# Performance work log

Measured on AMD Instinct MI355X. Metric: run time of the kernel, lower is better.

The kernel has to match this reference:

```python
import jax, jax.numpy as jnp
import numpy as np

TEMPERATURE = 0.2
EPS = 1e-10

def setup_inputs() -> dict:
    key = jax.random.key(0)
    x = jax.random.normal(key, (8, 1024, 64, 64), dtype=jnp.float32)
    return {"x": x}

def reference(x):
    B, C, H, W = x.shape
    xf = x.reshape(B, C, H * W)                      # [B, C, HW]
    dot = jnp.einsum('bcn,bdn->bcd', xf, xf) / TEMPERATURE  # [B, C, C]
    logits = jax.nn.softmax(dot, axis=-1)
    diag = jnp.diagonal(logits, axis1=-2, axis2=-1)  # [B, C]
    loss = -jnp.log(diag + EPS)
    return jnp.mean(loss)
```

## Files before the change

### kernel.cpp

```cpp
#include <hip/hip_runtime.h>
#include <hip/hip_bf16.h>

#define BATCH 8
#define CCH 1024
#define NHW 4096
#define SCALE 5.0f
#define ROWS (BATCH * CCH)

typedef unsigned char u8;
typedef unsigned int u32;
typedef __attribute__((ext_vector_type(4))) float float4v;
typedef __attribute__((ext_vector_type(4))) u32 uint4v;

__device__ __forceinline__ void async_load16(const void* gsrc, void* ldst) {
    __builtin_amdgcn_global_load_lds(
        (__attribute__((address_space(1))) void*)gsrc,
        (__attribute__((address_space(3))) void*)ldst,
        16, 0, 0);
}

__device__ __forceinline__ u32 pk4_fp8(float a, float b, float c, float d) {
    u32 v = __builtin_amdgcn_cvt_pk_fp8_f32(a, b, 0, false);
    v = __builtin_amdgcn_cvt_pk_fp8_f32(c, d, v, true);
    return v;
}

__device__ __forceinline__ float ssq4_fp8(u32 q) {
    float d0 = __builtin_amdgcn_cvt_f32_fp8(q, 0);
    float d1 = __builtin_amdgcn_cvt_f32_fp8(q, 1);
    float d2 = __builtin_amdgcn_cvt_f32_fp8(q, 2);
    float d3 = __builtin_amdgcn_cvt_f32_fp8(q, 3);
    return d0 * d0 + d1 * d1 + d2 * d2 + d3 * d3;
}

template <bool CONVERT>
__global__ __launch_bounds__(256) void prep_kernel(const float* __restrict__ x,
                                                   u8* __restrict__ xq,
                                                   float* __restrict__ diag,
                                                   float* __restrict__ l_acc) {
    const int row = blockIdx.x;
    const int tid = threadIdx.x;
    const float* src = x + (size_t)row * NHW;
    float ssum = 0.f;
#pragma unroll
    for (int p = 0; p < 4; ++p) {
        const int idx = p * 1024 + tid * 4;
        float4 v = *(const float4*)(src + idx);
        const u32 q = pk4_fp8(v.x, v.y, v.z, v.w);
        ssum += ssq4_fp8(q);
        if (CONVERT) *(u32*)(xq + (size_t)row * NHW + idx) = q;
    }
#pragma unroll
    for (int m = 1; m < 64; m <<= 1) ssum += __shfl_xor(ssum, m);
    __shared__ float red[4];
    if ((tid & 63) == 0) red[tid >> 6] = ssum;
    __syncthreads();
    if (tid == 0) {
        diag[row] = (red[0] + red[1] + red[2] + red[3]) * SCALE;
        l_acc[row] = 0.f;
    }
}

template <bool QSRC>
__global__ __launch_bounds__(256) void gram_kernel(const u8* __restrict__ Xq,
                                                   const float* __restrict__ Xf,
                                                   const float* __restrict__ diag,
                                                   float* __restrict__ l_acc,
                                                   float* __restrict__ num) {
    __shared__ __align__(16) u8 As[2][16384];
    __shared__ __align__(16) u8 Bs[2][8192];

    const int bid = blockIdx.x;
    const int b = bid & 7;
    const int t = bid >> 3;

    int bi = 0;
#pragma unroll
    for (int i = 7; i >= 1; --i) {
        if (t >= i * (17 - i)) { bi = i; break; }
    }
    const int bj2 = 2 * bi + (t - bi * (17 - bi));
    const bool aliasB = (bj2 == 2 * bi) || (bj2 == 2 * bi + 1);

    const int tid  = threadIdx.x;
    const int lane = tid & 63;
    const int w    = tid >> 6;
    const int wm   = w >> 1;
    const int wn   = w & 1;

    const int st_r  = lane >> 3;
    const int st_kc = (lane & 7) ^ st_r;

    const u8*    pA  = nullptr; const u8*    pB  = nullptr;
    const float* pAf = nullptr; const float* pBf = nullptr;
    if (QSRC) {
        const u8* baseX = Xq + (size_t)b * CCH * NHW;
        pA = baseX + (size_t)(bi * 128 + w * 32 + st_r) * NHW + st_kc * 16;
        pB = baseX + (size_t)(bj2 * 64 + w * 16 + st_r) * NHW + st_kc * 16;
    } else {
        const float* baseXf = Xf + (size_t)b * CCH * NHW;
        pAf = baseXf + (size_t)(bi * 128 + w * 32 + st_r) * NHW + st_kc * 16;
        pBf = baseXf + (size_t)(bj2 * 64 + w * 16 + st_r) * NHW + st_kc * 16;
    }

    float4v acc[4][2] = {};

    auto stage = [&](int buf, int K0) {
        if (QSRC) {
#pragma unroll
            for (int t8 = 0; t8 < 4; ++t8)
                async_load16(pA + (size_t)(t8 * 8) * NHW + K0,
                             As[buf] + (size_t)(w * 32 + t8 * 8) * 128);
            if (!aliasB) {
#pragma unroll
                for (int t8 = 0; t8 < 2; ++t8)
                    async_load16(pB + (size_t)(t8 * 8) * NHW + K0,
                                 Bs[buf] + (size_t)(w * 16 + t8 * 8) * 128);
            }
        } else {
#pragma unroll
            for (int t8 = 0; t8 < 4; ++t8) {
                const float* s = pAf + (size_t)(t8 * 8) * NHW + K0;
                float4 f0 = *(const float4*)(s);
                float4 f1 = *(const float4*)(s + 4);
                float4 f2 = *(const float4*)(s + 8);
                float4 f3 = *(const float4*)(s + 12);
                uint4v d;
                d.x = pk4_fp8(f0.x, f0.y, f0.z, f0.w);
                d.y = pk4_fp8(f1.x, f1.y, f1.z, f1.w);
                d.z = pk4_fp8(f2.x, f2.y, f2.z, f2.w);
                d.w = pk4_fp8(f3.x, f3.y, f3.z, f3.w);
                *(uint4v*)(As[buf] + (size_t)(w * 32 + t8 * 8 + st_r) * 128 + (lane & 7) * 16) = d;
            }
            if (!aliasB) {
#pragma unroll
                for (int t8 = 0; t8 < 2; ++t8) {
                    const float* s = pBf + (size_t)(t8 * 8) * NHW + K0;
                    float4 f0 = *(const float4*)(s);
                    float4 f1 = *(const float4*)(s + 4);
                    float4 f2 = *(const float4*)(s + 8);
                    float4 f3 = *(const float4*)(s + 12);
                    uint4v d;
                    d.x = pk4_fp8(f0.x, f0.y, f0.z, f0.w);
                    d.y = pk4_fp8(f1.x, f1.y, f1.z, f1.w);
                    d.z = pk4_fp8(f2.x, f2.y, f2.z, f2.w);
                    d.w = pk4_fp8(f3.x, f3.y, f3.z, f3.w);
                    *(uint4v*)(Bs[buf] + (size_t)(w * 16 + t8 * 8 + st_r) * 128 + (lane & 7) * 16) = d;
                }
            }
        }
    };

    stage(0, 0);
    __syncthreads();

    for (int i = 0; i < NHW / 128; ++i) {
        const int cur = i & 1;
        const int K0n = (i + 1) * 128;
        if (K0n < NHW) stage(cur ^ 1, K0n);

        const u8* Ab = As[cur];
        const u8* Bb = aliasB ? (Ab + (size_t)(bj2 - 2 * bi) * 64 * 128) : Bs[cur];
        const int q  = lane >> 4;
        const int rl = lane & 15;
#pragma unroll
        for (int s = 0; s < 4; ++s) {
            const int cbase = 2 * s + (q >> 1);
            const int boff  = (int)((cbase ^ (rl & 7)) * 16 + (q & 1) * 8);
            long af[4], bf[2];
#pragma unroll
            for (int mt = 0; mt < 4; ++mt)
                af[mt] = *(const long*)(Ab + (size_t)(wm * 64 + mt * 16 + rl) * 128 + boff);
#pragma unroll
            for (int nt = 0; nt < 2; ++nt)
                bf[nt] = *(const long*)(Bb + (size_t)(wn * 32 + nt * 16 + rl) * 128 + boff);
#pragma unroll
            for (int mt = 0; mt < 4; ++mt)
#pragma unroll
                for (int nt = 0; nt < 2; ++nt)
                    acc[mt][nt] = __builtin_amdgcn_mfma_f32_16x16x32_fp8_fp8(af[mt], bf[nt], acc[mt][nt], 0, 0, 0);
        }
        __syncthreads();
    }

    const int q  = lane >> 4;
    const int cl = lane & 15;
    const int rowbase = bi * 128 + wm * 64;
    const int colbase = bj2 * 64 + wn * 32;
    const float* dgb = diag + b * CCH;
    float* lb = l_acc + b * CCH;

#pragma unroll
    for (int mt = 0; mt < 4; ++mt) {
#pragma unroll
        for (int reg = 0; reg < 4; ++reg) {
            const int gr = rowbase + mt * 16 + q * 4 + reg;
            const float dg = dgb[gr];
            float s = 0.f;
#pragma unroll
            for (int nt = 0; nt < 2; ++nt) {
                const int gc = colbase + nt * 16 + cl;
                const float e = __expf(acc[mt][nt][reg] * SCALE - dg);
                if (gr <= gc) s += e;
                if (gr == gc) num[b * CCH + gr] = e;
            }
            s += __shfl_xor(s, 1);
            s += __shfl_xor(s, 2);
            s += __shfl_xor(s, 4);
            s += __shfl_xor(s, 8);
            if (cl == 0) atomicAdd(lb + gr, s);
        }
    }

#pragma unroll
    for (int nt = 0; nt < 2; ++nt) {
        const int gc = colbase + nt * 16 + cl;
        const float dgc = dgb[gc];
        float s = 0.f;
#pragma unroll
        for (int mt = 0; mt < 4; ++mt) {
#pragma unroll
            for (int reg = 0; reg < 4; ++reg) {
                const int gr = rowbase + mt * 16 + q * 4 + reg;
                if (gr < gc) s += __expf(acc[mt][nt][reg] * SCALE - dgc);
            }
        }
        s += __shfl_xor(s, 16);
        s += __shfl_xor(s, 32);
        if (lane < 16) atomicAdd(lb + gc, s);
    }
}

__global__ __launch_bounds__(1024) void finalize_kernel(const float* __restrict__ l_acc,
                                                        const float* __restrict__ num,
                                                        float* __restrict__ out) {
    const int tid = threadIdx.x;
    float s = 0.f;
    for (int r = tid; r < ROWS; r += 1024) {
        const float d = num[r] / l_acc[r];
        s += -__logf(d + 1e-10f);
    }
#pragma unroll
    for (int m = 1; m < 64; m <<= 1) s += __shfl_xor(s, m);
    __shared__ float red[16];
    if ((tid & 63) == 0) red[tid >> 6] = s;
    __syncthreads();
    if (tid == 0) {
        float tot = 0.f;
#pragma unroll
        for (int i = 0; i < 16; ++i) tot += red[i];
        out[0] = tot * (1.0f / (float)ROWS);
    }
}

extern "C" void kernel_launch(void* const* d_in, const int* in_sizes, int n_in,
                              void* d_out, int out_size, void* d_ws, size_t ws_size,
                              hipStream_t stream) {
    const float* x = (const float*)d_in[0];
    float* out = (float*)d_out;

    const size_t xq_bytes   = (size_t)BATCH * CCH * NHW;
    const size_t stat_bytes = (size_t)ROWS * 4;
    const bool fast = ws_size >= xq_bytes + 3 * stat_bytes;

    const int ntiles = 72;

    if (fast) {
        u8*    xq    = (u8*)d_ws;
        float* diag  = (float*)((char*)d_ws + xq_bytes);
        float* l_acc = diag + ROWS;
        float* num   = l_acc + ROWS;
        prep_kernel<true><<<ROWS, 256, 0, stream>>>(x, xq, diag, l_acc);
        gram_kernel<true><<<BATCH * ntiles, 256, 0, stream>>>(xq, nullptr, diag, l_acc, num);
        finalize_kernel<<<1, 1024, 0, stream>>>(l_acc, num, out);
    } else {
        float* diag  = (float*)d_ws;
        float* l_acc = diag + ROWS;
        float* num   = l_acc + ROWS;
        prep_kernel<false><<<ROWS, 256, 0, stream>>>(x, nullptr, diag, l_acc);
        gram_kernel<false><<<BATCH * ntiles, 256, 0, stream>>>(nullptr, x, diag, l_acc, num);
        finalize_kernel<<<1, 1024, 0, stream>>>(l_acc, num, out);
    }
}
```

Before: 241.0 us.

## Use persistent atomic-ticket gram kernel and fuse finalize via last-block reduction

The gram kernel becomes persistent: a fixed grid of 512 blocks pulls tile tickets from a global atomic counter until all 576 tiles are processed, instead of launching one block per tile. The separate finalize kernel is removed; the last block to finish, detected with a second counter and threadfences, computes the final mean loss. This is meant to cut one kernel launch and smooth load balance across the tail, at the cost of per-tile atomics and a serialized final reduction inside one block.

```diff
diff --git a/kernel.cpp b/kernel.cpp
--- a/kernel.cpp
+++ b/kernel.cpp
@@ -6,6 +6,9 @@
 #define NHW 4096
 #define SCALE 5.0f
 #define ROWS (BATCH * CCH)
+#define NTILES 72
+#define NTICK (BATCH * NTILES)
+#define GRID_G 512
 
 typedef unsigned char u8;
 typedef unsigned int u32;
@@ -37,7 +40,8 @@
 __global__ __launch_bounds__(256) void prep_kernel(const float* __restrict__ x,
                                                    u8* __restrict__ xq,
                                                    float* __restrict__ diag,
-                                                   float* __restrict__ l_acc) {
+                                                   float* __restrict__ l_acc,
+                                                   int* __restrict__ counters) {
     const int row = blockIdx.x;
     const int tid = threadIdx.x;
     const float* src = x + (size_t)row * NHW;
@@ -58,6 +62,7 @@
     if (tid == 0) {
         diag[row] = (red[0] + red[1] + red[2] + red[3]) * SCALE;
         l_acc[row] = 0.f;
+        if (row == 0) { counters[0] = 0; counters[1] = 0; }
     }
 }
 
@@ -66,21 +71,13 @@
                                                    const float* __restrict__ Xf,
                                                    const float* __restrict__ diag,
                                                    float* __restrict__ l_acc,
-                                                   float* __restrict__ num) {
+                                                   float* __restrict__ num,
+                                                   int* __restrict__ counters,
+                                                   float* __restrict__ out) {
     __shared__ __align__(16) u8 As[2][16384];
     __shared__ __align__(16) u8 Bs[2][8192];
-
-    const int bid = blockIdx.x;
-    const int b = bid & 7;
-    const int t = bid >> 3;
-
-    int bi = 0;
-#pragma unroll
-    for (int i = 7; i >= 1; --i) {
-        if (t >= i * (17 - i)) { bi = i; break; }
-    }
-    const int bj2 = 2 * bi + (t - bi * (17 - bi));
-    const bool aliasB = (bj2 == 2 * bi) || (bj2 == 2 * bi + 1);
+    __shared__ int s_ticket;
+    __shared__ float s_red[4];
 
     const int tid  = threadIdx.x;
     const int lane = tid & 63;
@@ -91,51 +88,53 @@
     const int st_r  = lane >> 3;
     const int st_kc = (lane & 7) ^ st_r;
 
-    const u8*    pA  = nullptr; const u8*    pB  = nullptr;
-    const float* pAf = nullptr; const float* pBf = nullptr;
-    if (QSRC) {
-        const u8* baseX = Xq + (size_t)b * CCH * NHW;
-        pA = baseX + (size_t)(bi * 128 + w * 32 + st_r) * NHW + st_kc * 16;
-        pB = baseX + (size_t)(bj2 * 64 + w * 16 + st_r) * NHW + st_kc * 16;
-    } else {
-        const float* baseXf = Xf + (size_t)b * CCH * NHW;
-        pAf = baseXf + (size_t)(bi * 128 + w * 32 + st_r) * NHW + st_kc * 16;
-        pBf = baseXf + (size_t)(bj2 * 64 + w * 16 + st_r) * NHW + st_kc * 16;
-    }
-
-    float4v acc[4][2] = {};
-
-    auto stage = [&](int buf, int K0) {
+    const int q_  = lane >> 4;
+    const int cl  = lane & 15;
+
+    for (;;) {
+        if (tid == 0) s_ticket = atomicAdd(counters + 0, 1);
+        __syncthreads();
+        const int tk = s_ticket;
+        if (tk >= NTICK) break;
+
+        const int b = tk & 7;
+        const int t = tk >> 3;
+        int bi = 0;
+#pragma unroll
+        for (int i = 7; i >= 1; --i) {
+            if (t >= i * (17 - i)) { bi = i; break; }
+        }
+        const int bj2 = 2 * bi + (t - bi * (17 - bi));
+        const bool aliasB = (bj2 == 2 * bi) || (bj2 == 2 * bi + 1);
+
+        const u8*    pA  = nullptr; const u8*    pB  = nullptr;
+        const float* pAf = nullptr; const float* pBf = nullptr;
         if (QSRC) {
-#pragma unroll
-            for (int t8 = 0; t8 < 4; ++t8)
-                async_load16(pA + (size_t)(t8 * 8) * NHW + K0,
-                             As[buf] + (size_t)(w * 32 + t8 * 8) * 128);
-            if (!aliasB) {
-#pragma unroll
-                for (int t8 = 0; t8 < 2; ++t8)
-                    async_load16(pB + (size_t)(t8 * 8) * NHW + K0,
-                                 Bs[buf] + (size_t)(w * 16 + t8 * 8) * 128);
-            }
+            const u8* baseX = Xq + (size_t)b * CCH * NHW;
+            pA = baseX + (size_t)(bi * 128 + w * 32 + st_r) * NHW + st_kc * 16;
+            pB = baseX + (size_t)(bj2 * 64 + w * 16 + st_r) * NHW + st_kc * 16;
         } else {
-#pragma unroll
-            for (int t8 = 0; t8 < 4; ++t8) {
-                const float* s = pAf + (size_t)(t8 * 8) * NHW + K0;
-                float4 f0 = *(const float4*)(s);
-                float4 f1 = *(const float4*)(s + 4);
-                float4 f2 = *(const float4*)(s + 8);
-                float4 f3 = *(const float4*)(s + 12);
-                uint4v d;
-                d.x = pk4_fp8(f0.x, f0.y, f0.z, f0.w);
-                d.y = pk4_fp8(f1.x, f1.y, f1.z, f1.w);
-                d.z = pk4_fp8(f2.x, f2.y, f2.z, f2.w);
-                d.w = pk4_fp8(f3.x, f3.y, f3.z, f3.w);
-                *(uint4v*)(As[buf] + (size_t)(w * 32 + t8 * 8 + st_r) * 128 + (lane & 7) * 16) = d;
-            }
-            if (!aliasB) {
-#pragma unroll
-                for (int t8 = 0; t8 < 2; ++t8) {
-                    const float* s = pBf + (size_t)(t8 * 8) * NHW + K0;
+            const float* baseXf = Xf + (size_t)b * CCH * NHW;
+            pAf = baseXf + (size_t)(bi * 128 + w * 32 + st_r) * NHW + st_kc * 16;
+            pBf = baseXf + (size_t)(bj2 * 64 + w * 16 + st_r) * NHW + st_kc * 16;
+        }
+
+        auto stage = [&](int buf, int K0) {
+            if (QSRC) {
+#pragma unroll
+                for (int t8 = 0; t8 < 4; ++t8)
+                    async_load16(pA + (size_t)(t8 * 8) * NHW + K0,
+                                 As[buf] + (size_t)(w * 32 + t8 * 8) * 128);
+                if (!aliasB) {
+#pragma unroll
+                    for (int t8 = 0; t8 < 2; ++t8)
+                        async_load16(pB + (size_t)(t8 * 8) * NHW + K0,
+                                     Bs[buf] + (size_t)(w * 16 + t8 * 8) * 128);
+                }
+            } else {
+#pragma unroll
+                for (int t8 = 0; t8 < 4; ++t8) {
+                    const float* s = pAf + (size_t)(t8 * 8) * NHW + K0;
                     float4 f0 = *(const float4*)(s);
                     float4 f1 = *(const float4*)(s + 4);
                     float4 f2 = *(const float4*)(s + 8);
@@ -145,111 +144,126 @@
                     d.y = pk4_fp8(f1.x, f1.y, f1.z, f1.w);
                     d.z = pk4_fp8(f2.x, f2.y, f2.z, f2.w);
                     d.w = pk4_fp8(f3.x, f3.y, f3.z, f3.w);
-                    *(uint4v*)(Bs[buf] + (size_t)(w * 16 + t8 * 8 + st_r) * 128 + (lane & 7) * 16) = d;
-                }
-            }
-        }
-    };
-
-    stage(0, 0);
-    __syncthreads();
-
-    for (int i = 0; i < NHW / 128; ++i) {
-        const int cur = i & 1;
-        const int K0n = (i + 1) * 128;
-        if (K0n < NHW) stage(cur ^ 1, K0n);
-
-        const u8* Ab = As[cur];
-        const u8* Bb = aliasB ? (Ab + (size_t)(bj2 - 2 * bi) * 64 * 128) : Bs[cur];
-        const int q  = lane >> 4;
-        const int rl = lane & 15;
-#pragma unroll
-        for (int s = 0; s < 4; ++s) {
-            const int cbase = 2 * s + (q >> 1);
-            const int boff  = (int)((cbase ^ (rl & 7)) * 16 + (q & 1) * 8);
-            long af[4], bf[2];
-#pragma unroll
-            for (int mt = 0; mt < 4; ++mt)
-                af[mt] = *(const long*)(Ab + (size_t)(wm * 64 + mt * 16 + rl) * 128 + boff);
-#pragma unroll
-            for (int nt = 0; nt < 2; ++nt)
-                bf[nt] = *(const long*)(Bb + (size_t)(wn * 32 + nt * 16 + rl) * 128 + boff);
-#pragma unroll
-            for (int mt = 0; mt < 4; ++mt)
+                    *(uint4v*)(As[buf] + (size_t)(w * 32 + t8 * 8 + st_r) * 128 + (lane & 7) * 16) = d;
+                }
+                if (!aliasB) {
+#pragma unroll
+                    for (int t8 = 0; t8 < 2; ++t8) {
+                        const float* s = pBf + (size_t)(t8 * 8) * NHW + K0;
+                        float4 f0 = *(const float4*)(s);
+                        float4 f1 = *(const float4*)(s + 4);
+                        float4 f2 = *(const float4*)(s + 8);
+                        float4 f3 = *(const float4*)(s + 12);
+                        uint4v d;
+                        d.x = pk4_fp8(f0.x, f0.y, f0.z, f0.w);
+                        d.y = pk4_fp8(f1.x, f1.y, f1.z, f1.w);
+                        d.z = pk4_fp8(f2.x, f2.y, f2.z, f2.w);
+                        d.w = pk4_fp8(f3.x, f3.y, f3.z, f3.w);
+                        *(uint4v*)(Bs[buf] + (size_t)(w * 16 + t8 * 8 + st_r) * 128 + (lane & 7) * 16) = d;
+                    }
+                }
+            }
+        };
+
+        float4v acc[4][2] = {};
+
+        stage(0, 0);
+        __syncthreads();
+
+        for (int i = 0; i < NHW / 128; ++i) {
+            const int cur = i & 1;
+            const int K0n = (i + 1) * 128;
+            if (K0n < NHW) stage(cur ^ 1, K0n);
+
+            const u8* Ab = As[cur];
+            const u8* Bb = aliasB ? (Ab + (size_t)(bj2 - 2 * bi) * 64 * 128) : Bs[cur];
+            const int rl = lane & 15;
+#pragma unroll
+            for (int s = 0; s < 4; ++s) {
+                const int cbase = 2 * s + (q_ >> 1);
+                const int boff  = (int)((cbase ^ (rl & 7)) * 16 + (q_ & 1) * 8);
+                long af[4], bf[2];
+#pragma unroll
+                for (int mt = 0; mt < 4; ++mt)
+                    af[mt] = *(const long*)(Ab + (size_t)(wm * 64 + mt * 16 + rl) * 128 + boff);
 #pragma unroll
                 for (int nt = 0; nt < 2; ++nt)
-                    acc[mt][nt] = __builtin_amdgcn_mfma_f32_16x16x32_fp8_fp8(af[mt], bf[nt], acc[mt][nt], 0, 0, 0);
-        }
-        __syncthreads();
-    }
-
-    const int q  = lane >> 4;
-    const int cl = lane & 15;
-    const int rowbase = bi * 128 + wm * 64;
-    const int colbase = bj2 * 64 + wn * 32;
-    const float* dgb = diag + b * CCH;
-    float* lb = l_acc + b * CCH;
-
-#pragma unroll
-    for (int mt = 0; mt < 4; ++mt) {
-#pragma unroll
-        for (int reg = 0; reg < 4; ++reg) {
-            const int gr = rowbase + mt * 16 + q * 4 + reg;
-            const float dg = dgb[gr];
+                    bf[nt] = *(const long*)(Bb + (size_t)(wn * 32 + nt * 16 + rl) * 128 + boff);
+#pragma unroll
+                for (int mt = 0; mt < 4; ++mt)
+#pragma unroll
+                    for (int nt = 0; nt < 2; ++nt)
+                        acc[mt][nt] = __builtin_amdgcn_mfma_f32_16x16x32_fp8_fp8(af[mt], bf[nt], acc[mt][nt], 0, 0, 0);
+            }
+            __syncthreads();
+        }
+
+        const int rowbase = bi * 128 + wm * 64;
+        const int colbase = bj2 * 64 + wn * 32;
+        const float* dgb = diag + b * CCH;
+        float* lb = l_acc + b * CCH;
+
+#pragma unroll
+        for (int mt = 0; mt < 4; ++mt) {
+#pragma unroll
+            for (int reg = 0; reg < 4; ++reg) {
+                const int gr = rowbase + mt * 16 + q_ * 4 + reg;
+                const float dg = dgb[gr];
+                float s = 0.f;
+#pragma unroll
+                for (int nt = 0; nt < 2; ++nt) {
+                    const int gc = colbase + nt * 16 + cl;
+                    const float e = __expf(acc[mt][nt][reg] * SCALE - dg);
+                    if (gr <= gc) s += e;
+                    if (gr == gc) num[b * CCH + gr] = e;
+                }
+                s += __shfl_xor(s, 1);
+                s += __shfl_xor(s, 2);
+                s += __shfl_xor(s, 4);
+                s += __shfl_xor(s, 8);
+                if (cl == 0) atomicAdd(lb + gr, s);
+            }
+        }
+
+#pragma unroll
+        for (int nt = 0; nt < 2; ++nt) {
+            const int gc = colbase + nt * 16 + cl;
+            const float dgc = dgb[gc];
             float s = 0.f;
 #pragma unroll
-            for (int nt = 0; nt < 2; ++nt) {
-                const int gc = colbase + nt * 16 + cl;
-                const float e = __expf(acc[mt][nt][reg] * SCALE - dg);
-                if (gr <= gc) s += e;
-                if (gr == gc) num[b * CCH + gr] = e;
-            }
-            s += __shfl_xor(s, 1);
-            s += __shfl_xor(s, 2);
-            s += __shfl_xor(s, 4);
-            s += __shfl_xor(s, 8);
-            if (cl == 0) atomicAdd(lb + gr, s);
-        }
-    }
-
-#pragma unroll
-    for (int nt = 0; nt < 2; ++nt) {
-        const int gc = colbase + nt * 16 + cl;
-        const float dgc = dgb[gc];
-        float s = 0.f;
-#pragma unroll
-        for (int mt = 0; mt < 4; ++mt) {
-#pragma unroll
-            for (int reg = 0; reg < 4; ++reg) {
-                const int gr = rowbase + mt * 16 + q * 4 + reg;
-                if (gr < gc) s += __expf(acc[mt][nt][reg] * SCALE - dgc);
-            }
-        }
-        s += __shfl_xor(s, 16);
-        s += __shfl_xor(s, 32);
-        if (lane < 16) atomicAdd(lb + gc, s);
-    }
-}
-
-__global__ __launch_bounds__(1024) void finalize_kernel(const float* __restrict__ l_acc,
-                                                        const float* __restrict__ num,
-                                                        float* __restrict__ out) {
-    const int tid = threadIdx.x;
-    float s = 0.f;
-    for (int r = tid; r < ROWS; r += 1024) {
-        const float d = num[r] / l_acc[r];
-        s += -__logf(d + 1e-10f);
-    }
-#pragma unroll
-    for (int m = 1; m < 64; m <<= 1) s += __shfl_xor(s, m);
-    __shared__ float red[16];
-    if ((tid & 63) == 0) red[tid >> 6] = s;
+            for (int mt = 0; mt < 4; ++mt) {
+#pragma unroll
+                for (int reg = 0; reg < 4; ++reg) {
+                    const int gr = rowbase + mt * 16 + q_ * 4 + reg;
+                    if (gr < gc) s += __expf(acc[mt][nt][reg] * SCALE - dgc);
+                }
+            }
+            s += __shfl_xor(s, 16);
+            s += __shfl_xor(s, 32);
+            if (lane < 16) atomicAdd(lb + gc, s);
+        }
+    }
+
     __syncthreads();
     if (tid == 0) {
-        float tot = 0.f;
-#pragma unroll
-        for (int i = 0; i < 16; ++i) tot += red[i];
-        out[0] = tot * (1.0f / (float)ROWS);
+        __threadfence();
+        const int old = atomicAdd(counters + 1, 1);
+        s_ticket = (old == GRID_G - 1) ? 1 : 0;
+    }
+    __syncthreads();
+    if (s_ticket) {
+        __threadfence();
+        float s = 0.f;
+        for (int r = tid; r < ROWS; r += 256) {
+            const float d = num[r] / l_acc[r];
+            s += -__logf(d + 1e-10f);
+        }
+#pragma unroll
+        for (int m = 1; m < 64; m <<= 1) s += __shfl_xor(s, m);
+        if ((tid & 63) == 0) s_red[tid >> 6] = s;
+        __syncthreads();
+        if (tid == 0)
+            out[0] = (s_red[0] + s_red[1] + s_red[2] + s_red[3]) * (1.0f / (float)ROWS);
     }
 }
 
@@ -261,24 +275,22 @@
 
     const size_t xq_bytes   = (size_t)BATCH * CCH * NHW;
     const size_t stat_bytes = (size_t)ROWS * 4;
-    const bool fast = ws_size >= xq_bytes + 3 * stat_bytes;
-
-    const int ntiles = 72;
+    const bool fast = ws_size >= xq_bytes + 3 * stat_bytes + 64;
 
     if (fast) {
         u8*    xq    = (u8*)d_ws;
         float* diag  = (float*)((char*)d_ws + xq_bytes);
         float* l_acc = diag + ROWS;
         float* num   = l_acc + ROWS;
-        prep_kernel<true><<<ROWS, 256, 0, stream>>>(x, xq, diag, l_acc);
-        gram_kernel<true><<<BATCH * ntiles, 256, 0, stream>>>(xq, nullptr, diag, l_acc, num);
-        finalize_kernel<<<1, 1024, 0, stream>>>(l_acc, num, out);
+        int*   cnt   = (int*)(num + ROWS);
+        prep_kernel<true><<<ROWS, 256, 0, stream>>>(x, xq, diag, l_acc, cnt);
+        gram_kernel<true><<<GRID_G, 256, 0, stream>>>(xq, nullptr, diag, l_acc, num, cnt, out);
     } else {
         float* diag  = (float*)d_ws;
         float* l_acc = diag + ROWS;
         float* num   = l_acc + ROWS;
-        prep_kernel<false><<<ROWS, 256, 0, stream>>>(x, nullptr, diag, l_acc);
-        gram_kernel<false><<<BATCH * ntiles, 256, 0, stream>>>(nullptr, x, diag, l_acc, num);
-        finalize_kernel<<<1, 1024, 0, stream>>>(l_acc, num, out);
-    }
-}
+        int*   cnt   = (int*)(num + ROWS);
+        prep_kernel<false><<<ROWS, 256, 0, stream>>>(x, nullptr, diag, l_acc, cnt);
+        gram_kernel<false><<<GRID_G, 256, 0, stream>>>(nullptr, x, diag, l_acc, num, cnt, out);
+    }
+}
```

Result: slower. 295.2 us (+22.5%).

## Triple-buffer gram kernel LDS staging with explicit vmcnt waits and single barrier

Applied to the files above, without the earlier changes.

Moves the FP8 gram kernel from double to triple buffering in LDS. It issues two stages ahead and replaces the two __syncthreads per iteration with a counted s_waitcnt on vector memory plus one s_barrier, so async global-to-LDS loads overlap more of the MFMA work. It also unrolls the finalize reduction into four independent accumulators. LDS use rises to 72KB per block, which may reduce occupancy. The hand-set waitcnt values only hold for the QSRC async path; the non-QSRC path converts and stores through registers, so its synchronization may be wrong.

```diff
diff --git a/kernel.cpp b/kernel.cpp
--- a/kernel.cpp
+++ b/kernel.cpp
@@ -6,11 +6,18 @@
 #define NHW 4096
 #define SCALE 5.0f
 #define ROWS (BATCH * CCH)
+#define NTILES 72
+#define GRID_G (BATCH * NTILES)
+#define KITERS (NHW / 128)
 
 typedef unsigned char u8;
 typedef unsigned int u32;
 typedef __attribute__((ext_vector_type(4))) float float4v;
 typedef __attribute__((ext_vector_type(4))) u32 uint4v;
+
+#define WAITCNT_VM0 0x0070
+#define WAITCNT_VM4 0x0074
+#define WAITCNT_VM6 0x0076
 
 __device__ __forceinline__ void async_load16(const void* gsrc, void* ldst) {
     __builtin_amdgcn_global_load_lds(
@@ -67,8 +74,8 @@
                                                    const float* __restrict__ diag,
                                                    float* __restrict__ l_acc,
                                                    float* __restrict__ num) {
-    __shared__ __align__(16) u8 As[2][16384];
-    __shared__ __align__(16) u8 Bs[2][8192];
+    __shared__ __align__(16) u8 As[3][16384];
+    __shared__ __align__(16) u8 Bs[3][8192];
 
     const int bid = blockIdx.x;
     const int b = bid & 7;
@@ -102,8 +109,6 @@
         pAf = baseXf + (size_t)(bi * 128 + w * 32 + st_r) * NHW + st_kc * 16;
         pBf = baseXf + (size_t)(bj2 * 64 + w * 16 + st_r) * NHW + st_kc * 16;
     }
-
-    float4v acc[4][2] = {};
 
     auto stage = [&](int buf, int K0) {
         if (QSRC) {
@@ -151,13 +156,28 @@
         }
     };
 
+    float4v acc[4][2] = {};
+
     stage(0, 0);
-    __syncthreads();
-
-    for (int i = 0; i < NHW / 128; ++i) {
-        const int cur = i & 1;
-        const int K0n = (i + 1) * 128;
-        if (K0n < NHW) stage(cur ^ 1, K0n);
+    stage(1, 128);
+
+    int cur = 0;
+    for (int i = 0; i < KITERS; ++i) {
+        __builtin_amdgcn_sched_barrier(0);
+        if (i == KITERS - 1) {
+            __builtin_amdgcn_s_waitcnt(WAITCNT_VM0);
+        } else if (aliasB) {
+            __builtin_amdgcn_s_waitcnt(WAITCNT_VM4);
+        } else {
+            __builtin_amdgcn_s_waitcnt(WAITCNT_VM6);
+        }
+        __builtin_amdgcn_s_barrier();
+        __builtin_amdgcn_sched_barrier(0);
+
+        if (i + 2 < KITERS) {
+            const int nx = (cur >= 1) ? cur - 1 : 2;
+            stage(nx, (i + 2) * 128);
+        }
 
         const u8* Ab = As[cur];
         const u8* Bb = aliasB ? (Ab + (size_t)(bj2 - 2 * bi) * 64 * 128) : Bs[cur];
@@ -180,11 +200,11 @@
                 for (int nt = 0; nt < 2; ++nt)
                     acc[mt][nt] = __builtin_amdgcn_mfma_f32_16x16x32_fp8_fp8(af[mt], bf[nt], acc[mt][nt], 0, 0, 0);
         }
-        __syncthreads();
-    }
-
-    const int q  = lane >> 4;
-    const int cl = lane & 15;
+        cur = (cur == 2) ? 0 : cur + 1;
+    }
+
+    const int q_  = lane >> 4;
+    const int cl  = lane & 15;
     const int rowbase = bi * 128 + wm * 64;
     const int colbase = bj2 * 64 + wn * 32;
     const float* dgb = diag + b * CCH;
@@ -194,7 +214,7 @@
     for (int mt = 0; mt < 4; ++mt) {
 #pragma unroll
         for (int reg = 0; reg < 4; ++reg) {
-            const int gr = rowbase + mt * 16 + q * 4 + reg;
+            const int gr = rowbase + mt * 16 + q_ * 4 + reg;
             const float dg = dgb[gr];
             float s = 0.f;
 #pragma unroll
@@ -221,7 +241,7 @@
         for (int mt = 0; mt < 4; ++mt) {
 #pragma unroll
             for (int reg = 0; reg < 4; ++reg) {
-                const int gr = rowbase + mt * 16 + q * 4 + reg;
+                const int gr = rowbase + mt * 16 + q_ * 4 + reg;
                 if (gr < gc) s += __expf(acc[mt][nt][reg] * SCALE - dgc);
             }
         }
@@ -235,11 +255,23 @@
                                                         const float* __restrict__ num,
                                                         float* __restrict__ out) {
     const int tid = threadIdx.x;
-    float s = 0.f;
-    for (int r = tid; r < ROWS; r += 1024) {
-        const float d = num[r] / l_acc[r];
-        s += -__logf(d + 1e-10f);
-    }
+    float s0 = 0.f, s1 = 0.f, s2 = 0.f, s3 = 0.f;
+#pragma unroll
+    for (int ib = 0; ib < 8; ib += 4) {
+        const int r0 = (ib + 0) * 1024 + tid;
+        const int r1 = (ib + 1) * 1024 + tid;
+        const int r2 = (ib + 2) * 1024 + tid;
+        const int r3 = (ib + 3) * 1024 + tid;
+        const float d0 = num[r0] / l_acc[r0];
+        const float d1 = num[r1] / l_acc[r1];
+        const float d2 = num[r2] / l_acc[r2];
+        const float d3 = num[r3] / l_acc[r3];
+        s0 += -__logf(d0 + 1e-10f);
+        s1 += -__logf(d1 + 1e-10f);
+        s2 += -__logf(d2 + 1e-10f);
+        s3 += -__logf(d3 + 1e-10f);
+    }
+    float s = (s0 + s1) + (s2 + s3);
 #pragma unroll
     for (int m = 1; m < 64; m <<= 1) s += __shfl_xor(s, m);
     __shared__ float red[16];
@@ -263,22 +295,20 @@
     const size_t stat_bytes = (size_t)ROWS * 4;
     const bool fast = ws_size >= xq_bytes + 3 * stat_bytes;
 
-    const int ntiles = 72;
-
     if (fast) {
         u8*    xq    = (u8*)d_ws;
         float* diag  = (float*)((char*)d_ws + xq_bytes);
         float* l_acc = diag + ROWS;
         float* num   = l_acc + ROWS;
         prep_kernel<true><<<ROWS, 256, 0, stream>>>(x, xq, diag, l_acc);
-        gram_kernel<true><<<BATCH * ntiles, 256, 0, stream>>>(xq, nullptr, diag, l_acc, num);
+        gram_kernel<true><<<GRID_G, 256, 0, stream>>>(xq, nullptr, diag, l_acc, num);
         finalize_kernel<<<1, 1024, 0, stream>>>(l_acc, num, out);
     } else {
         float* diag  = (float*)d_ws;
         float* l_acc = diag + ROWS;
         float* num   = l_acc + ROWS;
         prep_kernel<false><<<ROWS, 256, 0, stream>>>(x, nullptr, diag, l_acc);
-        gram_kernel<false><<<BATCH * ntiles, 256, 0, stream>>>(nullptr, x, diag, l_acc, num);
+        gram_kernel<false><<<GRID_G, 256, 0, stream>>>(nullptr, x, diag, l_acc, num);
         finalize_kernel<<<1, 1024, 0, stream>>>(l_acc, num, out);
     }
 }
```

Result: slower. 265.5 us (+10.2%).
